# Kernel tuning notes

Hardware: AMD Instinct MI355X
Metric: run time of the kernel (lower is better)

Reference implementation:

```python
import jax, jax.numpy as jnp
import numpy as np

B, S, HID = 2, 2048, 4096
N_HEADS, N_KV, HEAD_DIM = 32, 8, 128
N_REP = N_HEADS // N_KV
SCALING = HEAD_DIM ** -0.5
NEG_INF = -1e9


def setup_inputs() -> dict:
    key = jax.random.key(0)
    ks = jax.random.split(key, 6)
    hidden_states = jax.random.normal(ks[0], (B, S, HID), dtype=jnp.float32)
    # Real RoPE cos/sin (Llama, theta=10000): freqs repeated to full head_dim
    inv_freq = 1.0 / (10000.0 ** (jnp.arange(0, HEAD_DIM, 2, dtype=jnp.float32) / HEAD_DIM))
    pos = jnp.arange(S, dtype=jnp.float32)
    freqs = pos[:, None] * inv_freq[None, :]            # [S, HEAD_DIM//2]
    emb = jnp.concatenate([freqs, freqs], axis=-1)       # [S, HEAD_DIM]
    cos = jnp.broadcast_to(jnp.cos(emb)[None], (B, S, HEAD_DIM))
    sin = jnp.broadcast_to(jnp.sin(emb)[None], (B, S, HEAD_DIM))
    # Additive causal mask [B, 1, S, S]
    causal = jnp.triu(jnp.full((S, S), NEG_INF, dtype=jnp.float32), k=1)
    attention_mask = jnp.broadcast_to(causal[None, None], (B, 1, S, S))
    scale = 0.02
    wq = jax.random.normal(ks[1], (HID, N_HEADS * HEAD_DIM), dtype=jnp.float32) * scale
    wk = jax.random.normal(ks[2], (HID, N_KV * HEAD_DIM), dtype=jnp.float32) * scale
    wv = jax.random.normal(ks[3], (HID, N_KV * HEAD_DIM), dtype=jnp.float32) * scale
    wo = jax.random.normal(ks[4], (N_HEADS * HEAD_DIM, HID), dtype=jnp.float32) * scale
    return {"hidden_states": hidden_states, "cos": cos, "sin": sin,
            "attention_mask": attention_mask, "wq": wq, "wk": wk, "wv": wv, "wo": wo}


def _rotate_half(x):
    half = x.shape[-1] // 2
    return jnp.concatenate([-x[..., half:], x[..., :half]], axis=-1)


def reference(hidden_states, cos, sin, attention_mask, wq, wk, wv, wo):
    b, s, _ = hidden_states.shape
    # QKV projections (no bias)
    q = (hidden_states @ wq).reshape(b, s, N_HEADS, HEAD_DIM).transpose(0, 2, 1, 3)  # [b,H,s,d]
    k = (hidden_states @ wk).reshape(b, s, N_KV, HEAD_DIM).transpose(0, 2, 1, 3)     # [b,KV,s,d]
    v = (hidden_states @ wv).reshape(b, s, N_KV, HEAD_DIM).transpose(0, 2, 1, 3)
    # RoPE: broadcast cos/sin over heads (unsqueeze_dim=1)
    cos_e = cos[:, None, :, :]
    sin_e = sin[:, None, :, :]
    q = q * cos_e + _rotate_half(q) * sin_e
    k = k * cos_e + _rotate_half(k) * sin_e
    # repeat_kv: expand KV heads to match query heads
    k = jnp.repeat(k, N_REP, axis=1)  # [b,H,s,d]
    v = jnp.repeat(v, N_REP, axis=1)
    # Eager attention: full score matrix, fp32 softmax
    scores = jnp.einsum('bhqd,bhkd->bhqk', q, k) * SCALING + attention_mask
    weights = jax.nn.softmax(scores.astype(jnp.float32), axis=-1).astype(q.dtype)
    attn = jnp.einsum('bhqk,bhkd->bqhd', weights, v).reshape(b, s, N_HEADS * HEAD_DIM)
    return attn @ wo
```

## Files before the change

kernel.cpp:

```cpp
#include <hip/hip_runtime.h>
#include <hip/hip_bf16.h>

typedef __hip_bfloat16 bf16;
typedef __attribute__((ext_vector_type(8))) short short8;
typedef __attribute__((ext_vector_type(4))) float f32x4;

#define B_    2
#define S_    2048
#define HID_  4096
#define NH_   32
#define NKV_  8
#define HD_   128
#define QSTRIDE_ (NH_ * HD_)
#define QKVSTR_  6144
#define KOFF_    4096
#define VOFF_    5120
#define SCALE_ 0.08838834764831845f

__device__ __forceinline__ void lds_cp16(void* lds, const void* g) {
  __builtin_amdgcn_global_load_lds(
      (const __attribute__((address_space(1))) void*)g,
      (__attribute__((address_space(3))) void*)lds, 16, 0, 0);
}

__global__ void cvt_f32_bf16(const float* __restrict__ in, bf16* __restrict__ out,
                             long n) {
  const long i = ((long)blockIdx.x * blockDim.x + threadIdx.x) * 8;
  if (i >= n) return;
  float4 a = *(const float4*)(in + i);
  float4 b = *(const float4*)(in + i + 4);
  short8 cv;
  bf16 h;
  h = __float2bfloat16(a.x); cv[0] = *(short*)&h;
  h = __float2bfloat16(a.y); cv[1] = *(short*)&h;
  h = __float2bfloat16(a.z); cv[2] = *(short*)&h;
  h = __float2bfloat16(a.w); cv[3] = *(short*)&h;
  h = __float2bfloat16(b.x); cv[4] = *(short*)&h;
  h = __float2bfloat16(b.y); cv[5] = *(short*)&h;
  h = __float2bfloat16(b.z); cv[6] = *(short*)&h;
  h = __float2bfloat16(b.w); cv[7] = *(short*)&h;
  *(short8*)(out + i) = cv;
}

__global__ __launch_bounds__(256) void gemm_nt(const bf16* __restrict__ A,
                                               const bf16* __restrict__ Bt,
                                               bf16* __restrict__ C,
                                               int M, int N, int K) {
  __shared__ __align__(16) bf16 lA[128 * 32];
  __shared__ __align__(16) bf16 lB[128 * 32];
  const int tid  = threadIdx.x;
  const int wave = tid >> 6, lane = tid & 63;
  const int wm = wave >> 1, wn = wave & 1;
  const int quad = lane >> 4, l15 = lane & 15;
  const long m0 = (long)blockIdx.y * 128, n0 = (long)blockIdx.x * 128;
  const int srow = lane >> 2, scol = (lane & 3) * 8;
  f32x4 acc[4][4] = {};

  for (int k0 = 0; k0 < K; k0 += 32) {
    __syncthreads();
#pragma unroll
    for (int i = 0; i < 2; ++i) {
      const int c = wave * 2 + i;
      lds_cp16(&lA[c * 512], A  + (m0 + c * 16 + srow) * (long)K + k0 + scol);
      lds_cp16(&lB[c * 512], Bt + (n0 + c * 16 + srow) * (long)K + k0 + scol);
    }
    __syncthreads();
    short8 af[4], bq[4];
#pragma unroll
    for (int t = 0; t < 4; ++t)
      af[t] = *(const short8*)&lA[(wm * 64 + t * 16 + l15) * 32 + quad * 8];
#pragma unroll
    for (int t = 0; t < 4; ++t)
      bq[t] = *(const short8*)&lB[(wn * 64 + t * 16 + l15) * 32 + quad * 8];
#pragma unroll
    for (int tm = 0; tm < 4; ++tm)
#pragma unroll
      for (int tn = 0; tn < 4; ++tn)
        acc[tm][tn] = __builtin_amdgcn_mfma_f32_16x16x32_bf16(
            af[tm], bq[tn], acc[tm][tn], 0, 0, 0);
  }
#pragma unroll
  for (int tm = 0; tm < 4; ++tm)
#pragma unroll
    for (int tn = 0; tn < 4; ++tn)
#pragma unroll
      for (int r = 0; r < 4; ++r) {
        const long row = m0 + wm * 64 + tm * 16 + quad * 4 + r;
        const long col = n0 + wn * 64 + tn * 16 + l15;
        C[row * N + col] = __float2bfloat16(acc[tm][tn][r]);
      }
}

__global__ __launch_bounds__(256) void gemm_nt_f32(const bf16* __restrict__ A,
                                                   const bf16* __restrict__ Bt,
                                                   float* __restrict__ C,
                                                   int M, int N, int K) {
  __shared__ __align__(16) bf16 lA[128 * 32];
  __shared__ __align__(16) bf16 lB[128 * 32];
  const int tid  = threadIdx.x;
  const int wave = tid >> 6, lane = tid & 63;
  const int wm = wave >> 1, wn = wave & 1;
  const int quad = lane >> 4, l15 = lane & 15;
  const long m0 = (long)blockIdx.y * 128, n0 = (long)blockIdx.x * 128;
  const int srow = lane >> 2, scol = (lane & 3) * 8;
  f32x4 acc[4][4] = {};

  for (int k0 = 0; k0 < K; k0 += 32) {
    __syncthreads();
#pragma unroll
    for (int i = 0; i < 2; ++i) {
      const int c = wave * 2 + i;
      lds_cp16(&lA[c * 512], A  + (m0 + c * 16 + srow) * (long)K + k0 + scol);
      lds_cp16(&lB[c * 512], Bt + (n0 + c * 16 + srow) * (long)K + k0 + scol);
    }
    __syncthreads();
    short8 af[4], bq[4];
#pragma unroll
    for (int t = 0; t < 4; ++t)
      af[t] = *(const short8*)&lA[(wm * 64 + t * 16 + l15) * 32 + quad * 8];
#pragma unroll
    for (int t = 0; t < 4; ++t)
      bq[t] = *(const short8*)&lB[(wn * 64 + t * 16 + l15) * 32 + quad * 8];
#pragma unroll
    for (int tm = 0; tm < 4; ++tm)
#pragma unroll
      for (int tn = 0; tn < 4; ++tn)
        acc[tm][tn] = __builtin_amdgcn_mfma_f32_16x16x32_bf16(
            af[tm], bq[tn], acc[tm][tn], 0, 0, 0);
  }
#pragma unroll
  for (int tm = 0; tm < 4; ++tm)
#pragma unroll
    for (int tn = 0; tn < 4; ++tn)
#pragma unroll
      for (int r = 0; r < 4; ++r) {
        const long row = m0 + wm * 64 + tm * 16 + quad * 4 + r;
        const long col = n0 + wn * 64 + tn * 16 + l15;
        C[row * N + col] = acc[tm][tn][r];
      }
}

__global__ void transpose_f32_bf16(const float* __restrict__ in,
                                   bf16* __restrict__ out, int rows, int cols) {
  __shared__ bf16 t[32][33];
  const int c0 = blockIdx.x * 32, r0 = blockIdx.y * 32;
  const int tx = threadIdx.x, ty = threadIdx.y;
#pragma unroll
  for (int i = 0; i < 4; ++i)
    t[ty + i * 8][tx] =
        __float2bfloat16(in[(long)(r0 + ty + i * 8) * cols + c0 + tx]);
  __syncthreads();
#pragma unroll
  for (int i = 0; i < 4; ++i)
    out[(long)(c0 + ty + i * 8) * rows + r0 + tx] = t[tx][ty + i * 8];
}

__global__ void v_transpose(const bf16* __restrict__ QKV, bf16* __restrict__ VT) {
  __shared__ bf16 t[32][33];
  const int z = blockIdx.z;
  const int b = z >> 3, kv = z & 7;
  const int d0 = blockIdx.x * 32, s0 = blockIdx.y * 32;
  const int tx = threadIdx.x, ty = threadIdx.y;
#pragma unroll
  for (int i = 0; i < 4; ++i)
    t[ty + i * 8][tx] =
        QKV[(long)(b * S_ + s0 + ty + i * 8) * QKVSTR_ + VOFF_ + kv * HD_ + d0 + tx];
  __syncthreads();
#pragma unroll
  for (int i = 0; i < 4; ++i)
    VT[((long)z * HD_ + d0 + ty + i * 8) * S_ + s0 + tx] = t[tx][ty + i * 8];
}

__global__ void rope_kernel(bf16* __restrict__ x, const float* __restrict__ cosb,
                            const float* __restrict__ sinb, int nheads,
                            int stride, int off) {
  const int idx = blockIdx.x * blockDim.x + threadIdx.x;
  const int d  = idx & 63;
  const int h  = (idx >> 6) % nheads;
  const int bs = idx / (64 * nheads);
  if (bs >= B_ * S_) return;
  const long base = (long)bs * stride + off + h * HD_;
  const float x1 = __bfloat162float(x[base + d]);
  const float x2 = __bfloat162float(x[base + d + 64]);
  const float c1 = cosb[(long)bs * HD_ + d];
  const float c2 = cosb[(long)bs * HD_ + d + 64];
  const float s1 = sinb[(long)bs * HD_ + d];
  const float s2 = sinb[(long)bs * HD_ + d + 64];
  x[base + d]      = __float2bfloat16(x1 * c1 - x2 * s1);
  x[base + d + 64] = __float2bfloat16(x2 * c2 + x1 * s2);
}

__global__ __launch_bounds__(256, 2) void attn_fwd(const bf16* __restrict__ QKV,
                                                   const bf16* __restrict__ VT,
                                                   bf16* __restrict__ ctx) {
  __shared__ __align__(16) bf16 lK[64 * 128];
  __shared__ __align__(16) bf16 lV[128 * 64];
  __shared__ __align__(16) bf16 lP[128 * 64];
  const int tid  = threadIdx.x;
  const int wave = tid >> 6, lane = tid & 63;
  const int quad = lane >> 4, l15 = lane & 15;
  const int srow = lane >> 2, scol = (lane & 3) * 8;
  const int bh = blockIdx.y;
  const int b = bh >> 5, h = bh & 31, kv = h >> 2;
  const long qbase = (long)b * S_ * QKVSTR_ + h * HD_;
  const long kbase = (long)b * S_ * QKVSTR_ + KOFF_ + kv * HD_;
  const long vbase = (long)(b * NKV_ + kv) * HD_ * S_;
  const long cbase = (long)b * S_ * QSTRIDE_ + h * HD_;

  for (int pass = 0; pass < 2; ++pass) {
    const int qt = pass ? 15 - (int)blockIdx.x : (int)blockIdx.x;
    const int q0 = qt * 128;

    short8 qf[2][4];
#pragma unroll
    for (int mi = 0; mi < 2; ++mi)
#pragma unroll
      for (int kc = 0; kc < 4; ++kc)
        qf[mi][kc] = *(const short8*)(
            QKV + qbase + (long)(q0 + wave * 32 + mi * 16 + l15) * QKVSTR_ +
            kc * 32 + quad * 8);

    float lp[2][4] = {};
    f32x4 o[2][8] = {};

    const int nkt = 2 * qt + 2;
    for (int kt = 0; kt < nkt; ++kt) {
      const int k0 = kt * 64;
      __syncthreads();
#pragma unroll
      for (int i = 0; i < 4; ++i) {
        const int c = wave * 4 + i;
        lds_cp16(&lK[c * 512],
                 QKV + kbase + (long)(k0 + (c & 3) * 16 + srow) * QKVSTR_ +
                 (c >> 2) * 32 + scol);
        lds_cp16(&lV[c * 512],
                 VT + vbase + (long)((c & 7) * 16 + srow) * S_ + k0 +
                 (c >> 3) * 32 + scol);
      }
      __syncthreads();

      f32x4 sc[2][4] = {};
#pragma unroll
      for (int kc = 0; kc < 4; ++kc) {
        short8 kb[4];
#pragma unroll
        for (int j = 0; j < 4; ++j)
          kb[j] = *(const short8*)&lK[kc * 2048 + (j * 16 + l15) * 32 + quad * 8];
#pragma unroll
        for (int mi = 0; mi < 2; ++mi)
#pragma unroll
          for (int j = 0; j < 4; ++j)
            sc[mi][j] = __builtin_amdgcn_mfma_f32_16x16x32_bf16(
                qf[mi][kc], kb[j], sc[mi][j], 0, 0, 0);
      }

#pragma unroll
      for (int mi = 0; mi < 2; ++mi)
#pragma unroll
        for (int r = 0; r < 4; ++r) {
          const int qg = q0 + wave * 32 + mi * 16 + quad * 4 + r;
          const int rloc = wave * 32 + mi * 16 + quad * 4 + r;
#pragma unroll
          for (int j = 0; j < 4; ++j) {
            const int kg = k0 + j * 16 + l15;
            const float p = (kg <= qg) ? __expf(sc[mi][j][r] * SCALE_) : 0.f;
            lp[mi][r] += p;
            const int col = j * 16 + l15;
            lP[(col >> 5) * 4096 + rloc * 32 + (col & 31)] = __float2bfloat16(p);
          }
        }
      __syncthreads();

#pragma unroll
      for (int kc = 0; kc < 2; ++kc) {
        short8 pa[2];
#pragma unroll
        for (int mi = 0; mi < 2; ++mi)
          pa[mi] = *(const short8*)&lP[kc * 4096 + (wave * 32 + mi * 16 + l15) * 32 + quad * 8];
#pragma unroll
        for (int n = 0; n < 8; ++n) {
          const short8 vb = *(const short8*)&lV[kc * 4096 + (n * 16 + l15) * 32 + quad * 8];
#pragma unroll
          for (int mi = 0; mi < 2; ++mi)
            o[mi][n] = __builtin_amdgcn_mfma_f32_16x16x32_bf16(
                pa[mi], vb, o[mi][n], 0, 0, 0);
        }
      }
    }

#pragma unroll
    for (int mi = 0; mi < 2; ++mi)
#pragma unroll
      for (int r = 0; r < 4; ++r) {
        float l = lp[mi][r];
#pragma unroll
        for (int off = 1; off < 16; off <<= 1)
          l += __shfl_xor(l, off, 64);
        const float inv = 1.f / l;
        const long row = q0 + wave * 32 + mi * 16 + quad * 4 + r;
#pragma unroll
        for (int n = 0; n < 8; ++n)
          ctx[cbase + row * QSTRIDE_ + n * 16 + l15] =
              __float2bfloat16(o[mi][n][r] * inv);
      }
  }
}

extern "C" void kernel_launch(void* const* d_in, const int* in_sizes, int n_in,
                              void* d_out, int out_size, void* d_ws, size_t ws_size,
                              hipStream_t stream) {
  const float* hidden = (const float*)d_in[0];
  const float* cosb   = (const float*)d_in[1];
  const float* sinb   = (const float*)d_in[2];
  const float* wq = (const float*)d_in[4];
  const float* wk = (const float*)d_in[5];
  const float* wv = (const float*)d_in[6];
  const float* wo = (const float*)d_in[7];

  bf16* ws      = (bf16*)d_ws;
  bf16* hiddenB = ws;
  bf16* ctx     = ws;
  bf16* slotT   = ws + 16777216;
  bf16* VTb     = ws + 33554432;
  bf16* QKVb    = (bf16*)d_out;
  float* out    = (float*)d_out;

  const dim3 tb(32, 8);

  cvt_f32_bf16<<<8192, 256, 0, stream>>>(hidden, hiddenB, (long)B_ * S_ * HID_);

  transpose_f32_bf16<<<dim3(128, 128), tb, 0, stream>>>(wq, slotT, HID_, 4096);
  transpose_f32_bf16<<<dim3(32, 128), tb, 0, stream>>>(wk, slotT + (long)KOFF_ * HID_, HID_, 1024);
  transpose_f32_bf16<<<dim3(32, 128), tb, 0, stream>>>(wv, slotT + (long)VOFF_ * HID_, HID_, 1024);

  gemm_nt<<<dim3(48, 32), 256, 0, stream>>>(hiddenB, slotT, QKVb, B_ * S_, QKVSTR_, HID_);

  rope_kernel<<<(B_ * S_ * NH_ * 64) / 256, 256, 0, stream>>>(QKVb, cosb, sinb, NH_, QKVSTR_, 0);
  rope_kernel<<<(B_ * S_ * NKV_ * 64) / 256, 256, 0, stream>>>(QKVb, cosb, sinb, NKV_, QKVSTR_, KOFF_);

  v_transpose<<<dim3(4, 64, B_ * NKV_), tb, 0, stream>>>(QKVb, VTb);

  attn_fwd<<<dim3(8, B_ * NH_), 256, 0, stream>>>(QKVb, VTb, ctx);

  transpose_f32_bf16<<<dim3(128, 128), tb, 0, stream>>>(wo, slotT, QSTRIDE_, HID_);
  gemm_nt_f32<<<dim3(32, 32), 256, 0, stream>>>(ctx, slotT, out, B_ * S_, HID_, HID_);
}
```

Before: 824.4 us.

## Replace GEMMs with 256x256 tiles, double-buffered LDS prefetch, swizzle and XCD remap

Replaces both projection GEMM kernels with a shared templated 256x256-tile, 512-thread kernel. It uses a 64-wide K step, double-buffered LDS loaded with global_load_lds, an XOR swizzle to avoid bank conflicts, a staged interleave of MFMA with prefetch under s_setprio, and a workgroup index remap that spreads tiles across XCDs. The goal is to hide global-memory latency and raise MFMA utilisation and data reuse over the old single-buffered 128x128 kernel, which synchronised on every K step. In exchange the kernel needs 128KB of LDS and heavy register use, and the QKV GEMM launches far fewer blocks (384), which can hurt occupancy and wave balance.

New measurement: 766.2 us. -7.1%, faster.

```diff
diff --git a/kernel.cpp b/kernel.cpp
--- a/kernel.cpp
+++ b/kernel.cpp
@@ -42,102 +42,168 @@
   *(short8*)(out + i) = cv;
 }
 
-__global__ __launch_bounds__(256) void gemm_nt(const bf16* __restrict__ A,
-                                               const bf16* __restrict__ Bt,
-                                               bf16* __restrict__ C,
-                                               int M, int N, int K) {
-  __shared__ __align__(16) bf16 lA[128 * 32];
-  __shared__ __align__(16) bf16 lB[128 * 32];
+__device__ __forceinline__ void cstore(bf16* p, float v) { *p = __float2bfloat16(v); }
+__device__ __forceinline__ void cstore(float* p, float v) { *p = v; }
+
+template <typename CT>
+__device__ __forceinline__ void gemm256_body(bf16* L, const bf16* __restrict__ A,
+                                             const bf16* __restrict__ Bt,
+                                             CT* __restrict__ C, int M, int N,
+                                             int K) {
   const int tid  = threadIdx.x;
   const int wave = tid >> 6, lane = tid & 63;
-  const int wm = wave >> 1, wn = wave & 1;
+  const int wm = wave >> 2, wn = wave & 3;
   const int quad = lane >> 4, l15 = lane & 15;
-  const long m0 = (long)blockIdx.y * 128, n0 = (long)blockIdx.x * 128;
-  const int srow = lane >> 2, scol = (lane & 3) * 8;
-  f32x4 acc[4][4] = {};
-
-  for (int k0 = 0; k0 < K; k0 += 32) {
-    __syncthreads();
+  const int swz  = ((l15 >> 2) & 1) << 4;
+  const int srow = lane >> 3;
+  const int scol = ((lane & 7) << 3) ^ (((lane >> 5) & 1) << 4);
+
+  const int nbx = N >> 8;
+  const int nwg = nbx * (M >> 8);
+  int wg = (int)blockIdx.y * nbx + (int)blockIdx.x;
+  wg = (wg & 7) * (nwg >> 3) + (wg >> 3);
+  const long m0 = (long)(wg / nbx) << 8;
+  const long n0 = (long)(wg % nbx) << 8;
+  const int NT = K >> 6, HT = NT << 2;
+
+  auto STAGE = [&](int h) {
+    const int t = h >> 2, idx = h & 3;
+    const int isB = (idx >> 1) ^ 1;
+    bf16* region = L + (t & 1) * 32768 + isB * 16384 + (idx & 1) * 8192;
+    const bf16* src = isB ? Bt : A;
+    const long r0 = (isB ? n0 : m0) + (idx & 1) * 128 + srow;
+    const long gc = (long)t * 64 + scol;
 #pragma unroll
     for (int i = 0; i < 2; ++i) {
       const int c = wave * 2 + i;
-      lds_cp16(&lA[c * 512], A  + (m0 + c * 16 + srow) * (long)K + k0 + scol);
-      lds_cp16(&lB[c * 512], Bt + (n0 + c * 16 + srow) * (long)K + k0 + scol);
-    }
-    __syncthreads();
-    short8 af[4], bq[4];
-#pragma unroll
-    for (int t = 0; t < 4; ++t)
-      af[t] = *(const short8*)&lA[(wm * 64 + t * 16 + l15) * 32 + quad * 8];
-#pragma unroll
-    for (int t = 0; t < 4; ++t)
-      bq[t] = *(const short8*)&lB[(wn * 64 + t * 16 + l15) * 32 + quad * 8];
-#pragma unroll
-    for (int tm = 0; tm < 4; ++tm)
-#pragma unroll
-      for (int tn = 0; tn < 4; ++tn)
-        acc[tm][tn] = __builtin_amdgcn_mfma_f32_16x16x32_bf16(
-            af[tm], bq[tn], acc[tm][tn], 0, 0, 0);
-  }
-#pragma unroll
-  for (int tm = 0; tm < 4; ++tm)
-#pragma unroll
-    for (int tn = 0; tn < 4; ++tn)
+      lds_cp16(region + c * 512, src + (r0 + c * 8) * (long)K + gc);
+    }
+  };
+
+  f32x4 acc[8][4] = {};
+  short8 af[4][2];
+  short8 bfr[2][2][2];
+
+#pragma unroll
+  for (int h = 0; h < 6; ++h) STAGE(h);
+  asm volatile("s_waitcnt vmcnt(4)" ::: "memory");
+  __builtin_amdgcn_s_barrier();
+
+  auto TILE = [&](int t, int slot) {
+    const int abase = slot * 32768 + wm * 8192;
+    const int bbase = slot * 32768 + 16384 + (wn >> 1) * 8192 + (wn & 1) * 4096;
+    const int hb = 4 * t + 6;
+    const int c0 = (quad * 8) ^ swz;
+    const int c1 = (32 + quad * 8) ^ swz;
+
+#pragma unroll
+    for (int m = 0; m < 4; ++m) {
+      af[m][0] = *(const short8*)&L[abase + (m * 16 + l15) * 64 + c0];
+      af[m][1] = *(const short8*)&L[abase + (m * 16 + l15) * 64 + c1];
+    }
+#pragma unroll
+    for (int n = 0; n < 2; ++n) {
+      bfr[0][n][0] = *(const short8*)&L[bbase + (n * 16 + l15) * 64 + c0];
+      bfr[0][n][1] = *(const short8*)&L[bbase + (n * 16 + l15) * 64 + c1];
+    }
+    if (hb < HT) STAGE(hb);
+    __builtin_amdgcn_s_barrier();
+    asm volatile("s_waitcnt lgkmcnt(0)" ::: "memory");
+    __builtin_amdgcn_sched_barrier(0);
+    __builtin_amdgcn_s_setprio(1);
+#pragma unroll
+    for (int m = 0; m < 4; ++m)
+#pragma unroll
+      for (int n = 0; n < 2; ++n) {
+        acc[m][n] = __builtin_amdgcn_mfma_f32_16x16x32_bf16(af[m][0], bfr[0][n][0], acc[m][n], 0, 0, 0);
+        acc[m][n] = __builtin_amdgcn_mfma_f32_16x16x32_bf16(af[m][1], bfr[0][n][1], acc[m][n], 0, 0, 0);
+      }
+    __builtin_amdgcn_s_setprio(0);
+    __builtin_amdgcn_s_barrier();
+
+#pragma unroll
+    for (int n = 0; n < 2; ++n) {
+      bfr[1][n][0] = *(const short8*)&L[bbase + ((n + 2) * 16 + l15) * 64 + c0];
+      bfr[1][n][1] = *(const short8*)&L[bbase + ((n + 2) * 16 + l15) * 64 + c1];
+    }
+    if (hb + 1 < HT) STAGE(hb + 1);
+    __builtin_amdgcn_s_barrier();
+    asm volatile("s_waitcnt lgkmcnt(0)" ::: "memory");
+    __builtin_amdgcn_sched_barrier(0);
+    __builtin_amdgcn_s_setprio(1);
+#pragma unroll
+    for (int m = 0; m < 4; ++m)
+#pragma unroll
+      for (int n = 0; n < 2; ++n) {
+        acc[m][n + 2] = __builtin_amdgcn_mfma_f32_16x16x32_bf16(af[m][0], bfr[1][n][0], acc[m][n + 2], 0, 0, 0);
+        acc[m][n + 2] = __builtin_amdgcn_mfma_f32_16x16x32_bf16(af[m][1], bfr[1][n][1], acc[m][n + 2], 0, 0, 0);
+      }
+    __builtin_amdgcn_s_setprio(0);
+    __builtin_amdgcn_s_barrier();
+
+#pragma unroll
+    for (int m = 0; m < 4; ++m) {
+      af[m][0] = *(const short8*)&L[abase + (64 + m * 16 + l15) * 64 + c0];
+      af[m][1] = *(const short8*)&L[abase + (64 + m * 16 + l15) * 64 + c1];
+    }
+    if (hb + 2 < HT) STAGE(hb + 2);
+    __builtin_amdgcn_s_barrier();
+    asm volatile("s_waitcnt lgkmcnt(0)" ::: "memory");
+    __builtin_amdgcn_sched_barrier(0);
+    __builtin_amdgcn_s_setprio(1);
+#pragma unroll
+    for (int m = 0; m < 4; ++m)
+#pragma unroll
+      for (int n = 0; n < 2; ++n) {
+        acc[m + 4][n] = __builtin_amdgcn_mfma_f32_16x16x32_bf16(af[m][0], bfr[0][n][0], acc[m + 4][n], 0, 0, 0);
+        acc[m + 4][n] = __builtin_amdgcn_mfma_f32_16x16x32_bf16(af[m][1], bfr[0][n][1], acc[m + 4][n], 0, 0, 0);
+      }
+    __builtin_amdgcn_s_setprio(0);
+    __builtin_amdgcn_s_barrier();
+
+    if (hb + 3 < HT) STAGE(hb + 3);
+    __builtin_amdgcn_s_barrier();
+    __builtin_amdgcn_s_setprio(1);
+#pragma unroll
+    for (int m = 0; m < 4; ++m)
+#pragma unroll
+      for (int n = 0; n < 2; ++n) {
+        acc[m + 4][n + 2] = __builtin_amdgcn_mfma_f32_16x16x32_bf16(af[m][0], bfr[1][n][0], acc[m + 4][n + 2], 0, 0, 0);
+        acc[m + 4][n + 2] = __builtin_amdgcn_mfma_f32_16x16x32_bf16(af[m][1], bfr[1][n][1], acc[m + 4][n + 2], 0, 0, 0);
+      }
+    __builtin_amdgcn_s_setprio(0);
+    if (t < NT - 2) { asm volatile("s_waitcnt vmcnt(4)" ::: "memory"); }
+    else            { asm volatile("s_waitcnt vmcnt(0)" ::: "memory"); }
+    __builtin_amdgcn_s_barrier();
+  };
+
+#pragma unroll 1
+  for (int t = 0; t < NT; t += 2) { TILE(t, 0); TILE(t + 1, 1); }
+
+#pragma unroll
+  for (int mr = 0; mr < 8; ++mr)
+#pragma unroll
+    for (int nr = 0; nr < 4; ++nr)
 #pragma unroll
       for (int r = 0; r < 4; ++r) {
-        const long row = m0 + wm * 64 + tm * 16 + quad * 4 + r;
-        const long col = n0 + wn * 64 + tn * 16 + l15;
-        C[row * N + col] = __float2bfloat16(acc[tm][tn][r]);
-      }
-}
-
-__global__ __launch_bounds__(256) void gemm_nt_f32(const bf16* __restrict__ A,
-                                                   const bf16* __restrict__ Bt,
-                                                   float* __restrict__ C,
-                                                   int M, int N, int K) {
-  __shared__ __align__(16) bf16 lA[128 * 32];
-  __shared__ __align__(16) bf16 lB[128 * 32];
-  const int tid  = threadIdx.x;
-  const int wave = tid >> 6, lane = tid & 63;
-  const int wm = wave >> 1, wn = wave & 1;
-  const int quad = lane >> 4, l15 = lane & 15;
-  const long m0 = (long)blockIdx.y * 128, n0 = (long)blockIdx.x * 128;
-  const int srow = lane >> 2, scol = (lane & 3) * 8;
-  f32x4 acc[4][4] = {};
-
-  for (int k0 = 0; k0 < K; k0 += 32) {
-    __syncthreads();
-#pragma unroll
-    for (int i = 0; i < 2; ++i) {
-      const int c = wave * 2 + i;
-      lds_cp16(&lA[c * 512], A  + (m0 + c * 16 + srow) * (long)K + k0 + scol);
-      lds_cp16(&lB[c * 512], Bt + (n0 + c * 16 + srow) * (long)K + k0 + scol);
-    }
-    __syncthreads();
-    short8 af[4], bq[4];
-#pragma unroll
-    for (int t = 0; t < 4; ++t)
-      af[t] = *(const short8*)&lA[(wm * 64 + t * 16 + l15) * 32 + quad * 8];
-#pragma unroll
-    for (int t = 0; t < 4; ++t)
-      bq[t] = *(const short8*)&lB[(wn * 64 + t * 16 + l15) * 32 + quad * 8];
-#pragma unroll
-    for (int tm = 0; tm < 4; ++tm)
-#pragma unroll
-      for (int tn = 0; tn < 4; ++tn)
-        acc[tm][tn] = __builtin_amdgcn_mfma_f32_16x16x32_bf16(
-            af[tm], bq[tn], acc[tm][tn], 0, 0, 0);
-  }
-#pragma unroll
-  for (int tm = 0; tm < 4; ++tm)
-#pragma unroll
-    for (int tn = 0; tn < 4; ++tn)
-#pragma unroll
-      for (int r = 0; r < 4; ++r) {
-        const long row = m0 + wm * 64 + tm * 16 + quad * 4 + r;
-        const long col = n0 + wn * 64 + tn * 16 + l15;
-        C[row * N + col] = acc[tm][tn][r];
-      }
+        const long row = m0 + wm * 128 + mr * 16 + quad * 4 + r;
+        const long col = n0 + wn * 64 + nr * 16 + l15;
+        cstore(&C[row * (long)N + col], acc[mr][nr][r]);
+      }
+}
+
+__global__ __launch_bounds__(512, 2) void gemm256_bf16(
+    const bf16* __restrict__ A, const bf16* __restrict__ Bt,
+    bf16* __restrict__ C, int M, int N, int K) {
+  __shared__ __align__(16) bf16 L[65536];
+  gemm256_body<bf16>(L, A, Bt, C, M, N, K);
+}
+
+__global__ __launch_bounds__(512, 2) void gemm256_f32(
+    const bf16* __restrict__ A, const bf16* __restrict__ Bt,
+    float* __restrict__ C, int M, int N, int K) {
+  __shared__ __align__(16) bf16 L[65536];
+  gemm256_body<float>(L, A, Bt, C, M, N, K);
 }
 
 __global__ void transpose_f32_bf16(const float* __restrict__ in,
@@ -333,7 +399,8 @@
   transpose_f32_bf16<<<dim3(32, 128), tb, 0, stream>>>(wk, slotT + (long)KOFF_ * HID_, HID_, 1024);
   transpose_f32_bf16<<<dim3(32, 128), tb, 0, stream>>>(wv, slotT + (long)VOFF_ * HID_, HID_, 1024);
 
-  gemm_nt<<<dim3(48, 32), 256, 0, stream>>>(hiddenB, slotT, QKVb, B_ * S_, QKVSTR_, HID_);
+  gemm256_bf16<<<dim3(QKVSTR_ / 256, (B_ * S_) / 256), 512, 0, stream>>>(
+      hiddenB, slotT, QKVb, B_ * S_, QKVSTR_, HID_);
 
   rope_kernel<<<(B_ * S_ * NH_ * 64) / 256, 256, 0, stream>>>(QKVb, cosb, sinb, NH_, QKVSTR_, 0);
   rope_kernel<<<(B_ * S_ * NKV_ * 64) / 256, 256, 0, stream>>>(QKVb, cosb, sinb, NKV_, QKVSTR_, KOFF_);
@@ -343,5 +410,6 @@
   attn_fwd<<<dim3(8, B_ * NH_), 256, 0, stream>>>(QKVb, VTb, ctx);
 
   transpose_f32_bf16<<<dim3(128, 128), tb, 0, stream>>>(wo, slotT, QSTRIDE_, HID_);
-  gemm_nt_f32<<<dim3(32, 32), 256, 0, stream>>>(ctx, slotT, out, B_ * S_, HID_, HID_);
-}
+  gemm256_f32<<<dim3(HID_ / 256, (B_ * S_) / 256), 512, 0, stream>>>(
+      ctx, slotT, out, B_ * S_, HID_, HID_);
+}
```
